# Kernel optimization log

Measured on AMD Instinct MI355X. Metric: run time of the kernel, lower is better.

Reference implementation:

```python
import jax, jax.numpy as jnp
import numpy as np

B, C, H, W, D = 2, 512, 16, 16, 16
GROUPS = 32
EPS = 1e-6


def setup_inputs() -> dict:
    key = jax.random.key(0)
    ks = jax.random.split(key, 6)
    s = 1.0 / np.sqrt(C)
    inp = {
        "x": jax.random.normal(ks[0], (B, C, H, W, D), jnp.float32),
        "gn_w": jnp.ones((C,), jnp.float32),
        "gn_b": jnp.zeros((C,), jnp.float32),
        "wq": jax.random.normal(ks[1], (C, C), jnp.float32) * s,
        "bq": jnp.zeros((C,), jnp.float32),
        "wk": jax.random.normal(ks[2], (C, C), jnp.float32) * s,
        "bk": jnp.zeros((C,), jnp.float32),
        "wv": jax.random.normal(ks[3], (C, C), jnp.float32) * s,
        "bv": jnp.zeros((C,), jnp.float32),
        "wp": jax.random.normal(ks[4], (C, C), jnp.float32) * s,
        "bp": jnp.zeros((C,), jnp.float32),
    }
    return inp


def reference(x, gn_w, gn_b, wq, bq, wk, bk, wv, bv, wp, bp):
    b, c, h, w, d = x.shape
    # GroupNorm(32 groups, eps=1e-6, affine)
    xg = x.reshape(b, GROUPS, c // GROUPS, h, w, d)
    mu = xg.mean(axis=(2, 3, 4, 5), keepdims=True)
    var = xg.var(axis=(2, 3, 4, 5), keepdims=True)
    hn = ((xg - mu) / jnp.sqrt(var + EPS)).reshape(b, c, h, w, d)
    hn = hn * gn_w[None, :, None, None, None] + gn_b[None, :, None, None, None]
    # 1x1x1 conv projections == per-token channel matmul
    n = h * w * d
    hf = hn.reshape(b, c, n)
    q = jnp.einsum('oc,bcn->bon', wq, hf) + bq[None, :, None]  # [b,c,n]
    k = jnp.einsum('oc,bcn->bon', wk, hf) + bk[None, :, None]
    v = jnp.einsum('oc,bcn->bon', wv, hf) + bv[None, :, None]
    # attention: scores[b,i,j] = sum_c q[b,c,i] k[b,c,j] / sqrt(c)
    scores = jnp.einsum('bci,bcj->bij', q, k) * (c ** -0.5)
    attn = jax.nn.softmax(scores, axis=2)  # [b,n,n]
    # out[b,c,i] = sum_j v[b,c,j] attn[b,i,j]
    o = jnp.einsum('bij,bcj->bci', attn, v)
    o = jnp.einsum('oc,bcn->bon', wp, o) + bp[None, :, None]
    return x + o.reshape(b, c, h, w, d)
```

## Files before the change

### kernel.cpp

```cpp
#include <hip/hip_runtime.h>
#include <hip/hip_bf16.h>
#include <stdint.h>

typedef short short8 __attribute__((ext_vector_type(8)));
typedef float f32x4  __attribute__((ext_vector_type(4)));
typedef float f32x2  __attribute__((ext_vector_type(2)));
typedef float f32x16 __attribute__((ext_vector_type(16)));
typedef int   i32x4  __attribute__((ext_vector_type(4)));
typedef int   i32x8  __attribute__((ext_vector_type(8)));
typedef unsigned char uchar;

#define B_ 2
#define C_ 512
#define N_ 4096
#define G_ 32
#define WN (C_ * C_)
#define PREP_W 1024
#define PREP_BLOCKS 1030

static __device__ __forceinline__ short f2bf(float f) {
    return __builtin_bit_cast(short, __float2bfloat16(f));
}
static __device__ __forceinline__ uchar f2fp8(float f) {
    return (uchar)(__builtin_amdgcn_cvt_pk_fp8_f32(f, f, 0, false) & 0xff);
}
static __device__ __forceinline__ unsigned pk4fp8(float a, float b, float c, float d) {
    int w = __builtin_amdgcn_cvt_pk_fp8_f32(a, b, 0, false);
    w = __builtin_amdgcn_cvt_pk_fp8_f32(c, d, w, true);
    return (unsigned)w;
}

static __device__ __forceinline__ void async16(uchar* lds_wave_base, const uchar* g) {
    auto l  = (__attribute__((address_space(3))) unsigned int*)(uintptr_t)(lds_wave_base);
    auto gg = (const __attribute__((address_space(1))) unsigned int*)(g);
    __builtin_amdgcn_global_load_lds(gg, l, 16, 0, 0);
}

__global__ void prep_stats(const float* __restrict__ wq, const float* __restrict__ wk,
                           const float* __restrict__ wv, const float* __restrict__ wp,
                           const float* __restrict__ bq, const float* __restrict__ bk,
                           const float* __restrict__ bv,
                           const float* __restrict__ x,
                           uchar* __restrict__ Wb, float* __restrict__ bqkv,
                           float* __restrict__ raw) {
    if (blockIdx.x < PREP_W) {
        int i4 = blockIdx.x * 256 + threadIdx.x;
        int base = i4 * 4;
        int wsel = base >> 18;
        const float* src = (wsel == 0) ? wq : (wsel == 1) ? wk : (wsel == 2) ? wv : wp;
        float4 t = *(const float4*)(src + (base & (WN - 1)));
        ((unsigned*)Wb)[i4] = pk4fp8(t.x*16.f, t.y*16.f, t.z*16.f, t.w*16.f);
        return;
    }
    if (blockIdx.x < PREP_BLOCKS) {
        int j = (blockIdx.x - PREP_W) * 256 + threadIdx.x;
        if (j < 1536)
            bqkv[j] = (j < C_) ? bq[j] : (j < 2*C_) ? bk[j - C_] : bv[j - 2*C_];
        return;
    }
    const int idx = blockIdx.x - PREP_BLOCKS;
    const int bg = idx >> 2, qt = idx & 3;
    const float4* p = (const float4*)(x + (size_t)bg * 16 * N_ + (size_t)qt * 4 * N_);
    int tid = threadIdx.x;
    float s = 0.f, sq = 0.f;
    #pragma unroll
    for (int rep = 0; rep < 16; rep++) {
        float4 t = p[rep * 256 + tid];
        s  += t.x + t.y + t.z + t.w;
        sq += t.x*t.x + t.y*t.y + t.z*t.z + t.w*t.w;
    }
    __shared__ float rs[256], rq[256];
    rs[tid] = s; rq[tid] = sq;
    __syncthreads();
    for (int h = 128; h > 0; h >>= 1) {
        if (tid < h) { rs[tid] += rs[tid+h]; rq[tid] += rq[tid+h]; }
        __syncthreads();
    }
    if (tid == 0) {
        raw[idx*2+0] = rs[0];
        raw[idx*2+1] = rq[0];
    }
}

__global__ void gn_apply(const float* __restrict__ x, const float* __restrict__ raw,
                         const float* __restrict__ gw, const float* __restrict__ gb,
                         uchar* __restrict__ hn) {
    __shared__ uchar t[64 * 68];
    const int n0 = blockIdx.x * 64, c0 = blockIdx.y * 64, b = blockIdx.z;
    const int lane = threadIdx.x & 63, w = threadIdx.x >> 6;
    const float inv = 1.f / (16.f * N_);
    #pragma unroll
    for (int rep = 0; rep < 16; rep++) {
        int c  = rep * 4 + w;
        int cc = c0 + c;
        int g  = cc >> 4;
        int base = (b*G_ + g) * 8;
        float mean = (raw[base] + raw[base+2] + raw[base+4] + raw[base+6]) * inv;
        float var  = (raw[base+1] + raw[base+3] + raw[base+5] + raw[base+7]) * inv - mean * mean;
        float rstd = rsqrtf(var + 1e-6f);
        float sc = gw[cc] * rstd;
        float bi = gb[cc] - mean * sc;
        float v = x[((size_t)(b*C_ + cc)) * N_ + n0 + lane];
        t[lane*68 + c] = f2fp8(v * sc + bi);
    }
    __syncthreads();
    #pragma unroll
    for (int rep = 0; rep < 16; rep++) {
        int n = rep * 4 + w;
        hn[((size_t)(b*N_ + n0 + n)) * C_ + c0 + lane] = t[n*68 + lane];
    }
}

template<int BM, int BN, int BIAS_MODE, int OUT_MODE, int K, int SWZ>
__global__ __launch_bounds__(256, ((BM + BN) <= 256) ? 3 : 2)
void gemm_nt8(const uchar* __restrict__ A, int lda, long long sAz,
              const uchar* __restrict__ Bm, int ldb, long long sBz,
              void* __restrict__ Cv, int ldc, long long sCz,
              const float* __restrict__ bias,
              const void* __restrict__ resv,
              float alpha) {
    constexpr int MI = BM / 64;
    constexpr int NI = BN / 64;
    constexpr int AC = BM / 64;
    constexpr int BC = BN / 64;
    constexpr int T  = K / 64;
    constexpr int D  = (BM + BN) / 64;
    constexpr unsigned WAITD = 0xF70u | D;
    constexpr unsigned WAIT0 = 0xF70u;
    __shared__ uchar As[3][BM * 64];
    __shared__ uchar Bs[3][BN * 64];

    int bx, by, bz;
    if (SWZ == 1) {
        int fid = blockIdx.x;
        int xcd = fid & 7, j = fid >> 3;
        int gg = (j >> 2) * 8 + xcd;
        bx = j & 3; by = gg & 63; bz = gg >> 6;
    } else if (SWZ == 2) {
        int fid = blockIdx.x;
        int xcd = fid & 7, j = fid >> 3;
        bz = j >> 7;
        int r = j & 127;
        by = (xcd << 2) | (r >> 5);
        bx = r & 31;
    } else { bx = blockIdx.x; by = blockIdx.y; bz = blockIdx.z; }

    const int tid  = threadIdx.x;
    const int lane = tid & 63;
    const int wid  = tid >> 6;
    const int wr   = wid >> 1;
    const int wc   = wid & 1;
    const int m0 = by * BM;
    const int n0 = bx * BN;

    const int r  = tid >> 2;
    const int gc = (tid & 3) ^ ((r >> 1) & 3);
    const uchar* Ap = A  + sAz * bz + (size_t)(m0 + r) * lda + gc * 16;
    const uchar* Bp = Bm + sBz * bz + (size_t)(n0 + r) * ldb + gc * 16;

    f32x16 acc[MI][NI];
    #pragma unroll
    for (int i = 0; i < MI; i++)
        #pragma unroll
        for (int j = 0; j < NI; j++)
            #pragma unroll
            for (int e = 0; e < 16; e++)
                acc[i][j][e] = 0.f;

    f32x16 accs[MI];
    i32x8 ones8;
    if (OUT_MODE == 5) {
        #pragma unroll
        for (int i = 0; i < MI; i++)
            #pragma unroll
            for (int e = 0; e < 16; e++)
                accs[i][e] = 0.f;
        #pragma unroll
        for (int e = 0; e < 8; e++)
            ones8[e] = 0x38383838;
    }

    const int rl = lane & 31;
    const int hk = (lane >> 5) * 2;

    #define ISSUE(IB, u) do { size_t _kb = (size_t)(u) * 64; \
        _Pragma("unroll") \
        for (int c = 0; c < AC; c++) \
            async16(&As[IB][c * 4096 + wid * 1024], Ap + (size_t)c * 64 * lda + _kb); \
        _Pragma("unroll") \
        for (int c = 0; c < BC; c++) \
            async16(&Bs[IB][c * 4096 + wid * 1024], Bp + (size_t)c * 64 * ldb + _kb); } while (0)

    #define STEP(Bf, DO_ISSUE, IB, u, DO_BAR, WIMM) do { \
        i32x8 af[MI], bf[NI]; \
        _Pragma("unroll") \
        for (int i = 0; i < MI; i++) { \
            int ar = wr*(BM/2) + i*32 + rl; \
            int ao = ar*64 + ((hk ^ ((ar>>1)&3)) << 4); \
            *(i32x4*)&af[i]       = *(const i32x4*)&As[Bf][ao]; \
            *(((i32x4*)&af[i])+1) = *(const i32x4*)&As[Bf][ao ^ 16]; \
        } \
        _Pragma("unroll") \
        for (int i = 0; i < NI; i++) { \
            int br = wc*(BN/2) + i*32 + rl; \
            int bo = br*64 + ((hk ^ ((br>>1)&3)) << 4); \
            *(i32x4*)&bf[i]       = *(const i32x4*)&Bs[Bf][bo]; \
            *(((i32x4*)&bf[i])+1) = *(const i32x4*)&Bs[Bf][bo ^ 16]; \
        } \
        if (DO_ISSUE) ISSUE(IB, u); \
        _Pragma("unroll") \
        for (int mi = 0; mi < MI; mi++) \
            _Pragma("unroll") \
            for (int ni = 0; ni < NI; ni++) \
                acc[mi][ni] = __builtin_amdgcn_mfma_scale_f32_32x32x64_f8f6f4( \
                    af[mi], bf[ni], acc[mi][ni], 0, 0, 0, 127, 0, 127); \
        if (OUT_MODE == 5) { \
            _Pragma("unroll") \
            for (int mi = 0; mi < MI; mi++) \
                accs[mi] = __builtin_amdgcn_mfma_scale_f32_32x32x64_f8f6f4( \
                    af[mi], ones8, accs[mi], 0, 0, 0, 127, 0, 127); \
        } \
        if (DO_BAR) { __builtin_amdgcn_s_waitcnt(WIMM); __builtin_amdgcn_s_barrier(); } \
    } while (0)

    ISSUE(0, 0);
    ISSUE(1, 1);
    __builtin_amdgcn_s_waitcnt(WAITD);
    __builtin_amdgcn_s_barrier();

    constexpr int Gm = (T - 2) / 3;
    for (int m = 0; m < Gm; m++) {
        STEP(0, 1, 2, m*3 + 2, 1, WAITD);
        STEP(1, 1, 0, m*3 + 3, 1, WAITD);
        STEP(2, 1, 1, m*3 + 4, 1, WAITD);
    }
    if (T - 3*Gm == 2) {
        STEP(0, 0, 0, 0, 1, WAIT0);
        STEP(1, 0, 0, 0, 0, 0);
    } else {
        STEP(0, 1, 2, T-2, 1, WAITD);
        STEP(1, 1, 0, T-1, 1, WAITD);
        STEP(2, 0, 0, 0, 1, WAIT0);
        STEP(0, 0, 0, 0, 0, 0);
    }
    #undef ISSUE
    #undef STEP

    const int rh = (lane >> 5) * 4;

    if (OUT_MODE == 6) {
        #pragma unroll
        for (int mi = 0; mi < MI; mi++) {
            #pragma unroll
            for (int ni = 0; ni < NI; ni++) {
                int cc = n0 + wc*(BN/2) + ni*32 + rl;
                #pragma unroll
                for (int e = 0; e < 16; e++) {
                    int g = e >> 2, r4 = e & 3;
                    int rr = m0 + wr*(BM/2) + mi*32 + g*8 + rh + r4;
                    float p = fminf(__expf(acc[mi][ni][e] * alpha), 448.f);
                    long long idx = sCz * bz + (long long)rr * ldc + cc;
                    ((uchar*)Cv)[idx] = f2fp8(p);
                }
            }
        }
        return;
    }

    if (OUT_MODE == 5) {
        #pragma unroll
        for (int mi = 0; mi < MI; mi++) {
            #pragma unroll
            for (int e = 0; e < 16; e++) {
                int g = e >> 2, r4 = e & 3;
                int rr = m0 + wr*(BM/2) + mi*32 + g*8 + rh + r4;
                float rinv = __builtin_amdgcn_rcpf(accs[mi][e]) * alpha;
                #pragma unroll
                for (int ni = 0; ni < NI; ni++) {
                    int cc = n0 + wc*(BN/2) + ni*32 + rl;
                    long long idx = sCz * bz + (long long)rr * ldc + cc;
                    ((uchar*)Cv)[idx] = f2fp8(acc[mi][ni][e] * rinv);
                }
            }
        }
        return;
    }

    #pragma unroll
    for (int mi = 0; mi < MI; mi++) {
        #pragma unroll
        for (int ni = 0; ni < NI; ni++) {
            int cc = n0 + wc*(BN/2) + ni*32 + rl;
            float cb = (BIAS_MODE == 1) ? bias[cc] : 0.f;
            #pragma unroll
            for (int g = 0; g < 4; g++) {
                #pragma unroll
                for (int r4 = 0; r4 < 4; r4++) {
                    int rr = m0 + wr*(BM/2) + mi*32 + g*8 + rh + r4;
                    float val = acc[mi][ni][g*4 + r4] * alpha + cb;
                    if (BIAS_MODE == 2) val += bias[rr];
                    long long idx = sCz * bz + (long long)rr * ldc + cc;
                    if (OUT_MODE == 0)      ((short*)Cv)[idx] = f2bf(val);
                    else if (OUT_MODE == 2) ((float*)Cv)[idx] = val + ((const float*)resv)[idx];
                    else                    ((uchar*)Cv)[idx] = f2fp8(val);
                }
            }
        }
    }
}

extern "C" void kernel_launch(void* const* d_in, const int* in_sizes, int n_in,
                              void* d_out, int out_size, void* d_ws, size_t ws_size,
                              hipStream_t stream) {
    const float* x   = (const float*)d_in[0];
    const float* gnw = (const float*)d_in[1];
    const float* gnb = (const float*)d_in[2];
    const float* wq  = (const float*)d_in[3];
    const float* bq  = (const float*)d_in[4];
    const float* wk  = (const float*)d_in[5];
    const float* bk  = (const float*)d_in[6];
    const float* wv  = (const float*)d_in[7];
    const float* bv  = (const float*)d_in[8];
    const float* wp  = (const float*)d_in[9];
    const float* bp  = (const float*)d_in[10];
    float* out = (float*)d_out;
    char*  ws  = (char*)d_ws;

    float* raw  = (float*)(ws + 0);
    float* bqkv = (float*)(ws + 8192);
    uchar* Wb  = (uchar*)(ws + 65536);
    uchar* Hn  = (uchar*)(ws + (2ull  << 20));
    uchar* QK8 = (uchar*)(ws + (8ull  << 20));
    uchar* V8  = (uchar*)(ws + (16ull << 20));
    uchar* Ot8 = (uchar*)(ws + (20ull << 20));
    uchar* Sb  = (uchar*)(ws + (24ull << 20));

    prep_stats<<<PREP_BLOCKS + 256, 256, 0, stream>>>(wq, wk, wv, wp, bq, bk, bv, x,
                                                      Wb, bqkv, raw);
    gn_apply<<<dim3(N_/64, C_/64, B_), 256, 0, stream>>>(x, raw, gnw, gnb, Hn);

    const long long sHn = (long long)N_ * C_;
    const long long sQK = (long long)N_ * 1024;
    const long long sV  = (long long)C_ * N_;
    const long long sS  = (long long)N_ * N_;

    gemm_nt8<128,128,1,3,512,0><<<dim3(8, 32, 2), 256, 0, stream>>>(
        Hn, C_, sHn, Wb, C_, 0, QK8, 1024, sQK, bqkv, nullptr, 1.f/16.f);
    gemm_nt8<64,128,2,3,512,0><<<dim3(32, 8, 2), 256, 0, stream>>>(
        Wb + 2*WN, C_, 0, Hn, C_, sHn, V8, N_, sV, bv, nullptr, 1.f/16.f);

    gemm_nt8<128,128,0,6,512,2><<<2048, 256, 0, stream>>>(
        QK8, 1024, sQK, QK8 + 512, 1024, sQK, Sb, N_, sS, nullptr, nullptr,
        0.044194173824159216f);
    gemm_nt8<64,128,0,5,4096,1><<<512, 256, 0, stream>>>(
        Sb, N_, sS, V8, N_, sV, Ot8, C_, sHn, nullptr, nullptr, 16.f);
    gemm_nt8<64,128,2,2,512,0><<<dim3(32, 8, 2), 256, 0, stream>>>(
        Wb + 3*WN, C_, 0, Ot8, C_, sHn, out, N_, (long long)C_*N_, bp, x, 1.f/256.f);
}
```

Measured before the change: 169.9 us.

## Merge Q/K and V projection launches and add XCD-aware block swizzles

Refactors the GEMM template into a device-side body with caller-provided shared memory, then merges the QK and V projection GEMMs into one launch whose blocks pick their role by index. gn_apply, PV and the output projection now use XCD-aware 1D grid swizzles so neighbouring tiles land on the same chiplet and share L2. The aim is to cut one kernel launch, fill the machine better in the projection phase and improve L2 locality. The merged kernel sizes shared memory for the larger tile and uses a fixed occupancy bound, which may lower occupancy for the V-projection blocks.

Measured after the change: 167.6 us. About the same (-1.3%).

```diff
diff --git a/kernel.cpp b/kernel.cpp
--- a/kernel.cpp
+++ b/kernel.cpp
@@ -17,6 +17,11 @@
 #define WN (C_ * C_)
 #define PREP_W 1024
 #define PREP_BLOCKS 1030
+
+static constexpr long long sHn = (long long)N_ * C_;
+static constexpr long long sQK = (long long)N_ * 1024;
+static constexpr long long sV  = (long long)C_ * N_;
+static constexpr long long sS  = (long long)N_ * N_;
 
 static __device__ __forceinline__ short f2bf(float f) {
     return __builtin_bit_cast(short, __float2bfloat16(f));
@@ -86,7 +91,11 @@
                          const float* __restrict__ gw, const float* __restrict__ gb,
                          uchar* __restrict__ hn) {
     __shared__ uchar t[64 * 68];
-    const int n0 = blockIdx.x * 64, c0 = blockIdx.y * 64, b = blockIdx.z;
+    const int fid = blockIdx.x;
+    const int xcd = fid & 7, j = fid >> 3;
+    const int n0 = ((xcd << 3) | (j & 7)) * 64;
+    const int c0 = ((j >> 3) & 7) * 64;
+    const int b  = j >> 6;
     const int lane = threadIdx.x & 63, w = threadIdx.x >> 6;
     const float inv = 1.f / (16.f * N_);
     #pragma unroll
@@ -111,14 +120,16 @@
     }
 }
 
-template<int BM, int BN, int BIAS_MODE, int OUT_MODE, int K, int SWZ>
-__global__ __launch_bounds__(256, ((BM + BN) <= 256) ? 3 : 2)
-void gemm_nt8(const uchar* __restrict__ A, int lda, long long sAz,
-              const uchar* __restrict__ Bm, int ldb, long long sBz,
-              void* __restrict__ Cv, int ldc, long long sCz,
-              const float* __restrict__ bias,
-              const void* __restrict__ resv,
-              float alpha) {
+template<int BM, int BN, int BIAS_MODE, int OUT_MODE, int K>
+static __device__ __forceinline__ void gemm_body(
+        uchar* As_, uchar* Bs_,
+        int bx, int by, int bz,
+        const uchar* __restrict__ A, int lda, long long sAz,
+        const uchar* __restrict__ Bm, int ldb, long long sBz,
+        void* __restrict__ Cv, int ldc, long long sCz,
+        const float* __restrict__ bias,
+        const void* __restrict__ resv,
+        float alpha) {
     constexpr int MI = BM / 64;
     constexpr int NI = BN / 64;
     constexpr int AC = BM / 64;
@@ -127,23 +138,7 @@
     constexpr int D  = (BM + BN) / 64;
     constexpr unsigned WAITD = 0xF70u | D;
     constexpr unsigned WAIT0 = 0xF70u;
-    __shared__ uchar As[3][BM * 64];
-    __shared__ uchar Bs[3][BN * 64];
-
-    int bx, by, bz;
-    if (SWZ == 1) {
-        int fid = blockIdx.x;
-        int xcd = fid & 7, j = fid >> 3;
-        int gg = (j >> 2) * 8 + xcd;
-        bx = j & 3; by = gg & 63; bz = gg >> 6;
-    } else if (SWZ == 2) {
-        int fid = blockIdx.x;
-        int xcd = fid & 7, j = fid >> 3;
-        bz = j >> 7;
-        int r = j & 127;
-        by = (xcd << 2) | (r >> 5);
-        bx = r & 31;
-    } else { bx = blockIdx.x; by = blockIdx.y; bz = blockIdx.z; }
+    constexpr int ASZ = BM * 64, BSZ = BN * 64;
 
     const int tid  = threadIdx.x;
     const int lane = tid & 63;
@@ -186,10 +181,10 @@
     #define ISSUE(IB, u) do { size_t _kb = (size_t)(u) * 64; \
         _Pragma("unroll") \
         for (int c = 0; c < AC; c++) \
-            async16(&As[IB][c * 4096 + wid * 1024], Ap + (size_t)c * 64 * lda + _kb); \
+            async16(As_ + (IB)*ASZ + c * 4096 + wid * 1024, Ap + (size_t)c * 64 * lda + _kb); \
         _Pragma("unroll") \
         for (int c = 0; c < BC; c++) \
-            async16(&Bs[IB][c * 4096 + wid * 1024], Bp + (size_t)c * 64 * ldb + _kb); } while (0)
+            async16(Bs_ + (IB)*BSZ + c * 4096 + wid * 1024, Bp + (size_t)c * 64 * ldb + _kb); } while (0)
 
     #define STEP(Bf, DO_ISSUE, IB, u, DO_BAR, WIMM) do { \
         i32x8 af[MI], bf[NI]; \
@@ -197,15 +192,15 @@
         for (int i = 0; i < MI; i++) { \
             int ar = wr*(BM/2) + i*32 + rl; \
             int ao = ar*64 + ((hk ^ ((ar>>1)&3)) << 4); \
-            *(i32x4*)&af[i]       = *(const i32x4*)&As[Bf][ao]; \
-            *(((i32x4*)&af[i])+1) = *(const i32x4*)&As[Bf][ao ^ 16]; \
+            *(i32x4*)&af[i]       = *(const i32x4*)(As_ + (Bf)*ASZ + ao); \
+            *(((i32x4*)&af[i])+1) = *(const i32x4*)(As_ + (Bf)*ASZ + (ao ^ 16)); \
         } \
         _Pragma("unroll") \
         for (int i = 0; i < NI; i++) { \
             int br = wc*(BN/2) + i*32 + rl; \
             int bo = br*64 + ((hk ^ ((br>>1)&3)) << 4); \
-            *(i32x4*)&bf[i]       = *(const i32x4*)&Bs[Bf][bo]; \
-            *(((i32x4*)&bf[i])+1) = *(const i32x4*)&Bs[Bf][bo ^ 16]; \
+            *(i32x4*)&bf[i]       = *(const i32x4*)(Bs_ + (Bf)*BSZ + bo); \
+            *(((i32x4*)&bf[i])+1) = *(const i32x4*)(Bs_ + (Bf)*BSZ + (bo ^ 16)); \
         } \
         if (DO_ISSUE) ISSUE(IB, u); \
         _Pragma("unroll") \
@@ -309,6 +304,66 @@
     }
 }
 
+__global__ __launch_bounds__(256, 2)
+void qkv_kernel(const uchar* __restrict__ Hn, const uchar* __restrict__ Wb,
+                uchar* __restrict__ QK8, uchar* __restrict__ V8,
+                const float* __restrict__ bqkv) {
+    __shared__ uchar smem[49152];
+    int fid = blockIdx.x;
+    if (fid < 512) {
+        int xcd = fid & 7, j = fid >> 3;
+        int by = (xcd << 2) | (j & 3);
+        int bx = (j >> 2) & 7, bz = j >> 5;
+        gemm_body<128,128,1,3,512>(smem, smem + 3*128*64, bx, by, bz,
+            Hn, C_, sHn, Wb, C_, 0, QK8, 1024, sQK, bqkv, nullptr, 1.f/16.f);
+    } else {
+        int f2 = fid - 512;
+        int xcd = f2 & 7, j = f2 >> 3;
+        int bx = (xcd << 2) | (j & 3);
+        int by = (j >> 2) & 7, bz = j >> 5;
+        gemm_body<64,128,2,3,512>(smem, smem + 3*64*64, bx, by, bz,
+            Wb + 2*WN, C_, 0, Hn, C_, sHn, V8, N_, sV, bqkv + 1024, nullptr, 1.f/16.f);
+    }
+}
+
+__global__ __launch_bounds__(256, 2)
+void s_kernel(const uchar* __restrict__ QK8, uchar* __restrict__ Sb, float alpha) {
+    __shared__ uchar smem[49152];
+    int fid = blockIdx.x;
+    int xcd = fid & 7, j = fid >> 3;
+    int bz = j >> 7;
+    int r = j & 127;
+    int by = (xcd << 2) | (r >> 5);
+    int bx = r & 31;
+    gemm_body<128,128,0,6,512>(smem, smem + 3*128*64, bx, by, bz,
+        QK8, 1024, sQK, QK8 + 512, 1024, sQK, Sb, N_, sS, nullptr, nullptr, alpha);
+}
+
+__global__ __launch_bounds__(256, 3)
+void pv_kernel(const uchar* __restrict__ Sb, const uchar* __restrict__ V8,
+               uchar* __restrict__ Ot8) {
+    __shared__ uchar smem[36864];
+    int fid = blockIdx.x;
+    int xcd = fid & 7, j = fid >> 3;
+    int by = (xcd << 3) | (j & 7);
+    int bx = (j >> 3) & 3, bz = j >> 5;
+    gemm_body<64,128,0,5,4096>(smem, smem + 3*64*64, bx, by, bz,
+        Sb, N_, sS, V8, N_, sV, Ot8, C_, sHn, nullptr, nullptr, 16.f);
+}
+
+__global__ __launch_bounds__(256, 3)
+void proj_kernel(const uchar* __restrict__ Wb3, const uchar* __restrict__ Ot8,
+                 const float* __restrict__ x, const float* __restrict__ bp,
+                 float* __restrict__ out) {
+    __shared__ uchar smem[36864];
+    int fid = blockIdx.x;
+    int xcd = fid & 7, j = fid >> 3;
+    int bx = (xcd << 2) | (j & 3);
+    int by = (j >> 2) & 7, bz = j >> 5;
+    gemm_body<64,128,2,2,512>(smem, smem + 3*64*64, bx, by, bz,
+        Wb3, C_, 0, Ot8, C_, sHn, out, N_, (long long)C_ * N_, bp, x, 1.f/256.f);
+}
+
 extern "C" void kernel_launch(void* const* d_in, const int* in_sizes, int n_in,
                               void* d_out, int out_size, void* d_ws, size_t ws_size,
                               hipStream_t stream) {
@@ -337,23 +392,13 @@
 
     prep_stats<<<PREP_BLOCKS + 256, 256, 0, stream>>>(wq, wk, wv, wp, bq, bk, bv, x,
                                                       Wb, bqkv, raw);
-    gn_apply<<<dim3(N_/64, C_/64, B_), 256, 0, stream>>>(x, raw, gnw, gnb, Hn);
-
-    const long long sHn = (long long)N_ * C_;
-    const long long sQK = (long long)N_ * 1024;
-    const long long sV  = (long long)C_ * N_;
-    const long long sS  = (long long)N_ * N_;
-
-    gemm_nt8<128,128,1,3,512,0><<<dim3(8, 32, 2), 256, 0, stream>>>(
-        Hn, C_, sHn, Wb, C_, 0, QK8, 1024, sQK, bqkv, nullptr, 1.f/16.f);
-    gemm_nt8<64,128,2,3,512,0><<<dim3(32, 8, 2), 256, 0, stream>>>(
-        Wb + 2*WN, C_, 0, Hn, C_, sHn, V8, N_, sV, bv, nullptr, 1.f/16.f);
-
-    gemm_nt8<128,128,0,6,512,2><<<2048, 256, 0, stream>>>(
-        QK8, 1024, sQK, QK8 + 512, 1024, sQK, Sb, N_, sS, nullptr, nullptr,
-        0.044194173824159216f);
-    gemm_nt8<64,128,0,5,4096,1><<<512, 256, 0, stream>>>(
-        Sb, N_, sS, V8, N_, sV, Ot8, C_, sHn, nullptr, nullptr, 16.f);
-    gemm_nt8<64,128,2,2,512,0><<<dim3(32, 8, 2), 256, 0, stream>>>(
-        Wb + 3*WN, C_, 0, Ot8, C_, sHn, out, N_, (long long)C_*N_, bp, x, 1.f/256.f);
-}
+    gn_apply<<<1024, 256, 0, stream>>>(x, raw, gnw, gnb, Hn);
+
+    qkv_kernel<<<1024, 256, 0, stream>>>(Hn, Wb, QK8, V8, bqkv);
+
+    s_kernel<<<2048, 256, 0, stream>>>(QK8, Sb, 0.044194173824159216f);
+
+    pv_kernel<<<512, 256, 0, stream>>>(Sb, V8, Ot8);
+
+    proj_kernel<<<512, 256, 0, stream>>>(Wb + 3*WN, Ot8, x, bp, out);
+}
```
